# Kernel optimization log

Hardware: AMD Instinct MI355X
Metric: run time of the kernel (lower is better)

Reference implementation:

```python
import jax, jax.numpy as jnp
import numpy as np

B, N = 8192, 128          # batch, num intruders
D_OWN, D_GRID, D_INTR = 16, 512, 20
H, OUT = 128, 4


def setup_inputs() -> dict:
    key = jax.random.key(0)
    ks = jax.random.split(key, 12)
    rn = lambda k, shape, s=1.0: jax.random.normal(k, shape, jnp.float32) * s
    return {
        "state0": rn(ks[0], (B, D_OWN)),
        "state1": rn(ks[1], (B, D_GRID)),
        "state2": rn(ks[2], (B, N, D_INTR)),
        "W_own": rn(ks[3], (D_OWN, H), 0.1), "b_own": jnp.zeros((H,), jnp.float32),
        "W_intr": rn(ks[4], (D_INTR, H), 0.1), "b_intr": jnp.zeros((H,), jnp.float32),
        "W_grid": rn(ks[5], (D_GRID, H), 0.05), "b_grid": jnp.zeros((H,), jnp.float32),
        "Wq": rn(ks[6], (H, H), 0.08),
        "Wk": rn(ks[7], (H, H), 0.08),
        "Wv": rn(ks[8], (H, H), 0.08),
        "W1": rn(ks[9], (3 * H, H), 0.05), "b1": jnp.zeros((H,), jnp.float32),
        "W2": rn(ks[10], (H, OUT), 0.1), "b2": jnp.zeros((OUT,), jnp.float32),
    }


def reference(state0, state1, state2, W_own, b_own, W_intr, b_intr,
              W_grid, b_grid, Wq, Wk, Wv, W1, b1, W2, b2):
    own_e = jax.nn.relu(state0 @ W_own + b_own)            # [B,H]
    x_e = jax.nn.relu(state2 @ W_intr + b_intr)            # [B,N,H]
    q = own_e @ Wq                                         # [B,H]
    k = x_e @ Wk                                           # [B,N,H]
    v = x_e @ Wv                                           # [B,N,H]
    # mask = state2.mean(axis=2, keepdim=True).bool()  (nonzero test)
    mask = jnp.mean(state2, axis=2, keepdims=True) != 0    # [B,N,1]
    score = jnp.einsum('bnh,bh->bn', k, q)[..., None]      # bmm(k, q.unsqueeze(2)) -> [B,N,1]
    score = jnp.where(mask, score, -jnp.inf)
    alpha = jax.nn.softmax(score / np.float32(np.sqrt(H)), axis=1)
    alpha = jnp.where(mask, alpha, 0.0)
    v_att = jnp.sum(v * alpha, axis=1)                     # [B,H]
    own_grid = jax.nn.relu(state1 @ W_grid + b_grid)       # [B,H]
    concat = jnp.concatenate([own_e, v_att, own_grid], axis=1)  # [B,3H]
    out = (concat @ W1 + b1) @ W2 + b2                     # action_out_SAC
    mean = out
    log_std = jnp.clip(out, -20.0, 2.0)
    return mean, log_std
```

## Files before the change

### kernel.cpp

```cpp
#include <hip/hip_runtime.h>

typedef unsigned short ushort_t;
typedef __attribute__((ext_vector_type(8))) short bf16x8;
typedef __attribute__((ext_vector_type(4))) float f32x4;

__device__ __forceinline__ float bflo(unsigned u) { return __uint_as_float(u << 16); }
__device__ __forceinline__ float bfhi(unsigned u) { return __uint_as_float(u & 0xffff0000u); }
__device__ __forceinline__ float bfu(ushort_t s)  { return __uint_as_float((unsigned)s << 16); }
__device__ __forceinline__ ushort_t f2bf(float f) {
    unsigned u = __float_as_uint(f);
    u = u + 0x7fffu + ((u >> 16) & 1u);
    return (ushort_t)(u >> 16);
}
__device__ __forceinline__ void unpack8(uint4 v, float* f) {
    f[0]=bflo(v.x); f[1]=bfhi(v.x); f[2]=bflo(v.y); f[3]=bfhi(v.y);
    f[4]=bflo(v.z); f[5]=bfhi(v.z); f[6]=bflo(v.w); f[7]=bfhi(v.w);
}

__device__ __forceinline__ float load1(const void* p, size_t i, int f32) {
    return f32 ? ((const float*)p)[i] : bfu(((const ushort_t*)p)[i]);
}
__device__ __forceinline__ void load8(const void* p, size_t i, int f32, float* f) {
    if (f32) {
        const float4 a = *(const float4*)((const float*)p + i);
        const float4 b = *(const float4*)((const float*)p + i + 4);
        f[0]=a.x; f[1]=a.y; f[2]=a.z; f[3]=a.w;
        f[4]=b.x; f[5]=b.y; f[6]=b.z; f[7]=b.w;
    } else {
        unpack8(*(const uint4*)((const ushort_t*)p + i), f);
    }
}
__device__ __forceinline__ void load4(const void* p, size_t i, int f32, float* f) {
    if (f32) {
        const float4 a = *(const float4*)((const float*)p + i);
        f[0]=a.x; f[1]=a.y; f[2]=a.z; f[3]=a.w;
    } else {
        const uint2 u = *(const uint2*)((const ushort_t*)p + i);
        f[0]=bflo(u.x); f[1]=bfhi(u.x); f[2]=bflo(u.y); f[3]=bfhi(u.y);
    }
}

__device__ __forceinline__ int detect_f32(const ushort_t* s1h) {
    const int ln = threadIdx.x & 63;
    float v = fmaxf(fabsf(bfu(s1h[ln])), fabsf(bfu(s1h[ln + 64])));
    bool big = !(v <= 1e6f);
    return __ballot(big) != 0ull;
}

#define B_TOT 8192

__device__ __attribute__((aligned(16))) float    g_M[128 * 128];
__device__ __attribute__((aligned(16))) float    g_Wc1[384 * 4];
__device__ __attribute__((aligned(16))) float    g_Wv2[128 * 4];
__device__ __attribute__((aligned(16))) float    g_bc[4];
__device__ __attribute__((aligned(16))) float    g_t[B_TOT * 128];
__device__ __attribute__((aligned(16))) float    g_ogc[B_TOT * 4];
__device__ __attribute__((aligned(16))) ushort_t g_oe[B_TOT * 128];

__global__ __launch_bounds__(128) void k_pre(
    const void* __restrict__ Wq, const void* __restrict__ Wk,
    const void* __restrict__ Wv, const void* __restrict__ W1,
    const void* __restrict__ b1, const void* __restrict__ W2,
    const void* __restrict__ b2, const ushort_t* __restrict__ s1h)
{
    __shared__ float wq_sh[128];
    __shared__ float w2_sh[512];
    __shared__ float wc1_mid[512];
    __shared__ float redc[128][4];
    const int tid = threadIdx.x;
    const int bx = blockIdx.x;
    const int f32 = detect_f32(s1h);

    if (bx < 128) {
        wq_sh[tid] = load1(Wq, bx*128 + tid, f32);
        __syncthreads();
        float acc = 0.f;
        #pragma unroll
        for (int c = 0; c < 16; ++c) {
            float f[8]; load8(Wk, (size_t)tid*128 + c*8, f32, f);
            #pragma unroll
            for (int j = 0; j < 8; ++j) acc = fmaf(wq_sh[c*8+j], f[j], acc);
        }
        g_M[bx*128 + tid] = acc;
    } else {
        const int rbase = (bx == 128) ? 0 : ((bx == 129) ? 128 : 256);
        for (int i = tid; i < 512; i += 128) w2_sh[i] = load1(W2, i, f32);
        __syncthreads();

        const int r = rbase + tid;
        float a[4] = {0.f, 0.f, 0.f, 0.f};
        #pragma unroll
        for (int c = 0; c < 16; ++c) {
            float f[8]; load8(W1, (size_t)r*128 + c*8, f32, f);
            #pragma unroll
            for (int j = 0; j < 8; ++j) {
                const int p = c*8 + j;
                #pragma unroll
                for (int q = 0; q < 4; ++q) a[q] = fmaf(f[j], w2_sh[p*4+q], a[q]);
            }
        }
        #pragma unroll
        for (int q = 0; q < 4; ++q) g_Wc1[r*4+q] = a[q];

        if (bx == 129) {
            #pragma unroll
            for (int q = 0; q < 4; ++q) wc1_mid[tid*4+q] = a[q];
            __syncthreads();
            float v[4] = {0.f, 0.f, 0.f, 0.f};
            #pragma unroll
            for (int c = 0; c < 16; ++c) {
                float f[8]; load8(Wv, (size_t)tid*128 + c*8, f32, f);
                #pragma unroll
                for (int j = 0; j < 8; ++j) {
                    const int i2 = c*8 + j;
                    #pragma unroll
                    for (int q = 0; q < 4; ++q) v[q] = fmaf(f[j], wc1_mid[i2*4+q], v[q]);
                }
            }
            #pragma unroll
            for (int q = 0; q < 4; ++q) g_Wv2[tid*4+q] = v[q];

            const float bv = load1(b1, tid, f32);
            #pragma unroll
            for (int q = 0; q < 4; ++q) redc[tid][q] = bv * w2_sh[tid*4+q];
            __syncthreads();
            for (int s = 64; s > 0; s >>= 1) {
                if (tid < s) {
                    #pragma unroll
                    for (int q = 0; q < 4; ++q) redc[tid][q] += redc[tid+s][q];
                }
                __syncthreads();
            }
            if (tid < 4) g_bc[tid] = redc[0][tid] + load1(b2, tid, f32);
        }
    }
}

__global__ __launch_bounds__(256) void k_ownt(
    const void* __restrict__ state0, const void* __restrict__ W_own,
    const void* __restrict__ b_own, const ushort_t* __restrict__ s1h)
{
    __shared__ float s0sh[16*16];
    __shared__ float wosh[16*128];
    __shared__ float bosh[128];
    __shared__ float oesh[16*129];
    __shared__ float Mt[32][128];
    const int tid = threadIdx.x;
    const int b0 = blockIdx.x * 16;
    const int f32 = detect_f32(s1h);

    if (tid < 32) {
        float f[8]; load8(state0, (size_t)b0*16 + tid*8, f32, f);
        #pragma unroll
        for (int j = 0; j < 8; ++j) s0sh[tid*8 + j] = f[j];
    }
    {
        float f[8]; load8(W_own, (size_t)tid*8, f32, f);
        #pragma unroll
        for (int j = 0; j < 8; ++j) wosh[tid*8 + j] = f[j];
    }
    if (tid < 128) bosh[tid] = load1(b_own, tid, f32);
    __syncthreads();

    #pragma unroll
    for (int kk = 0; kk < 8; ++kk) {
        const int idx = tid + kk*256;
        const int bi = idx >> 7, h = idx & 127;
        float acc = bosh[h];
        #pragma unroll
        for (int d = 0; d < 16; ++d) acc = fmaf(s0sh[bi*16+d], wosh[d*128+h], acc);
        acc = fmaxf(acc, 0.f);
        oesh[bi*129 + h] = acc;
        g_oe[(size_t)(b0+bi)*128 + h] = f2bf(acc);
    }

    const int bi0 = (tid >> 5) * 2;
    const int h0  = (tid & 31) * 4;
    float t00=0.f,t01=0.f,t02=0.f,t03=0.f,t10=0.f,t11=0.f,t12=0.f,t13=0.f;
    for (int kt = 0; kt < 128; kt += 32) {
        __syncthreads();
        #pragma unroll
        for (int c = 0; c < 4; ++c) {
            const int i = tid + c*256;
            const int kk = i >> 5;
            const int hh = (i & 31) * 4;
            *(float4*)&Mt[kk][hh] = *(const float4*)&g_M[(size_t)(kt+kk)*128 + hh];
        }
        __syncthreads();
        #pragma unroll
        for (int k = 0; k < 32; ++k) {
            const float4 mv = *(const float4*)&Mt[k][h0];
            const float a0 = oesh[(bi0+0)*129 + kt + k];
            const float a1 = oesh[(bi0+1)*129 + kt + k];
            t00=fmaf(a0,mv.x,t00); t01=fmaf(a0,mv.y,t01); t02=fmaf(a0,mv.z,t02); t03=fmaf(a0,mv.w,t03);
            t10=fmaf(a1,mv.x,t10); t11=fmaf(a1,mv.y,t11); t12=fmaf(a1,mv.z,t12); t13=fmaf(a1,mv.w,t13);
        }
    }
    *(float4*)&g_t[(size_t)(b0+bi0+0)*128 + h0] = make_float4(t00,t01,t02,t03);
    *(float4*)&g_t[(size_t)(b0+bi0+1)*128 + h0] = make_float4(t10,t11,t12,t13);
}

__global__ __launch_bounds__(256) void k_grid(
    const void* __restrict__ state1, const void* __restrict__ W_grid,
    const void* __restrict__ b_grid)
{
    __shared__ float s1T[32][18];
    __shared__ float wg[32][128];
    __shared__ float part[32][16][4];
    const int tid = threadIdx.x;
    const int b0 = blockIdx.x * 16;
    const int f32 = detect_f32((const ushort_t*)state1);

    const int bq = tid & 7;
    const int hq = tid >> 3;
    float a00=0.f,a01=0.f,a02=0.f,a03=0.f;
    float a10=0.f,a11=0.f,a12=0.f,a13=0.f;

    for (int kt = 0; kt < 512; kt += 32) {
        if (kt) __syncthreads();
        if (tid < 128) {
            const int bb = tid >> 3;
            const int kk = (tid & 7) * 4;
            float f[4];
            load4(state1, (size_t)(b0 + bb)*512 + kt + kk, f32, f);
            #pragma unroll
            for (int j = 0; j < 4; ++j) s1T[kk + j][bb] = f[j];
        }
        {
            #pragma unroll
            for (int c = 0; c < 4; ++c) {
                const int i = tid + c*256;
                const int kk = i >> 5;
                const int hh = (i & 31) * 4;
                float f[4];
                load4(W_grid, (size_t)(kt + kk)*128 + hh, f32, f);
                *(float4*)&wg[kk][hh] = make_float4(f[0], f[1], f[2], f[3]);
            }
        }
        __syncthreads();
        #pragma unroll 8
        for (int k = 0; k < 32; ++k) {
            const float x0 = s1T[k][bq*2 + 0];
            const float x1 = s1T[k][bq*2 + 1];
            const float4 w = *(const float4*)&wg[k][hq*4];
            a00=fmaf(x0,w.x,a00); a01=fmaf(x0,w.y,a01); a02=fmaf(x0,w.z,a02); a03=fmaf(x0,w.w,a03);
            a10=fmaf(x1,w.x,a10); a11=fmaf(x1,w.y,a11); a12=fmaf(x1,w.z,a12); a13=fmaf(x1,w.w,a13);
        }
    }

    float accs[2][4] = {{a00,a01,a02,a03},{a10,a11,a12,a13}};
    float pr[2][4] = {{0,0,0,0},{0,0,0,0}};
    #pragma unroll
    for (int jh = 0; jh < 4; ++jh) {
        const int h = hq*4 + jh;
        const float bg = load1(b_grid, h, f32);
        const float4 wc = *(const float4*)&g_Wc1[(256 + h)*4];
        #pragma unroll
        for (int ib = 0; ib < 2; ++ib) {
            const float og = fmaxf(accs[ib][jh] + bg, 0.f);
            pr[ib][0] = fmaf(og, wc.x, pr[ib][0]);
            pr[ib][1] = fmaf(og, wc.y, pr[ib][1]);
            pr[ib][2] = fmaf(og, wc.z, pr[ib][2]);
            pr[ib][3] = fmaf(og, wc.w, pr[ib][3]);
        }
    }
    __syncthreads();
    #pragma unroll
    for (int j = 0; j < 4; ++j) {
        part[hq][bq*2+0][j] = pr[0][j];
        part[hq][bq*2+1][j] = pr[1][j];
    }
    __syncthreads();
    if (tid < 64) {
        const int bb = tid >> 2, j = tid & 3;
        float s = 0.f;
        #pragma unroll
        for (int q = 0; q < 32; ++q) s += part[q][bb][j];
        g_ogc[(size_t)(b0 + bb)*4 + j] = s;
    }
}

__global__ __launch_bounds__(256) void k_main(
    const void* __restrict__ state2, const void* __restrict__ W_intr,
    const void* __restrict__ b_intr, const ushort_t* __restrict__ s1h,
    void* __restrict__ out_raw)
{
    __shared__ __attribute__((aligned(16))) ushort_t s2b[128*40];
    __shared__ __attribute__((aligned(16))) ushort_t wib[128*40];
    __shared__ float bi_sh[128], t_sh[128], oe_sh[128];
    __shared__ float score_sh[128], alpha_sh[128], u_sh[128];
    __shared__ float u_red[4][128];
    __shared__ int   msk_sh[128];
    __shared__ float red_sh[8];
    __shared__ float red4[4][4];

    const int tid = threadIdx.x;
    const int b = blockIdx.x;
    const int f32 = detect_f32(s1h);

    if (tid < 128) {
        const int n = tid;
        float v[20];
        const size_t base = (size_t)b*2560 + n*20;
        #pragma unroll
        for (int c = 0; c < 5; ++c) load4(state2, base + c*4, f32, v + c*4);
        float ms = 0.f;
        #pragma unroll
        for (int d = 0; d < 20; ++d) ms += v[d];
        msk_sh[n] = (ms != 0.f) ? 1 : 0;
        unsigned* row = (unsigned*)&s2b[n*40];
        #pragma unroll
        for (int c = 0; c < 10; ++c)
            row[c] = (unsigned)f2bf(v[2*c]) | ((unsigned)f2bf(v[2*c+1]) << 16);
        #pragma unroll
        for (int c = 10; c < 20; ++c) row[c] = 0u;
        t_sh[n]  = g_t[(size_t)b*128 + n];
        oe_sh[n] = bfu(g_oe[(size_t)b*128 + n]);
        bi_sh[n] = load1(b_intr, n, f32);
    } else {
        const int h = tid - 128;
        float w[20];
        #pragma unroll
        for (int d = 0; d < 20; ++d) w[d] = load1(W_intr, (size_t)d*128 + h, f32);
        unsigned* row = (unsigned*)&wib[h*40];
        #pragma unroll
        for (int c = 0; c < 10; ++c)
            row[c] = (unsigned)f2bf(w[2*c]) | ((unsigned)f2bf(w[2*c+1]) << 16);
        #pragma unroll
        for (int c = 10; c < 20; ++c) row[c] = 0u;
    }
    __syncthreads();

    const int wv = tid >> 6, ln = tid & 63, lq = ln >> 4, lc = ln & 15;
    const bf16x8 a0 = *(const bf16x8*)&s2b[((2*wv+0)*16 + lc)*40 + lq*8];
    const bf16x8 a1 = *(const bf16x8*)&s2b[((2*wv+1)*16 + lc)*40 + lq*8];
    const f32x4 zf = {0.f, 0.f, 0.f, 0.f};
    f32x4 acc[2][8];
    #pragma unroll
    for (int th = 0; th < 8; ++th) {
        const bf16x8 bb = *(const bf16x8*)&wib[(th*16 + lc)*40 + lq*8];
        acc[0][th] = __builtin_amdgcn_mfma_f32_16x16x32_bf16(a0, bb, zf, 0, 0, 0);
        acc[1][th] = __builtin_amdgcn_mfma_f32_16x16x32_bf16(a1, bb, zf, 0, 0, 0);
    }

    float sc[2][4] = {{0,0,0,0},{0,0,0,0}};
    #pragma unroll
    for (int th = 0; th < 8; ++th) {
        const float bh = bi_sh[th*16 + lc];
        const float tv = t_sh[th*16 + lc];
        #pragma unroll
        for (int i = 0; i < 2; ++i)
            #pragma unroll
            for (int r = 0; r < 4; ++r) {
                const float xv = fmaxf(acc[i][th][r] + bh, 0.f);
                acc[i][th][r] = xv;
                sc[i][r] = fmaf(xv, tv, sc[i][r]);
            }
    }
    #pragma unroll
    for (int off = 1; off < 16; off <<= 1)
        #pragma unroll
        for (int i = 0; i < 2; ++i)
            #pragma unroll
            for (int r = 0; r < 4; ++r)
                sc[i][r] += __shfl_xor(sc[i][r], off);
    if (lc == 0) {
        #pragma unroll
        for (int i = 0; i < 2; ++i)
            #pragma unroll
            for (int r = 0; r < 4; ++r)
                score_sh[(2*wv+i)*16 + lq*4 + r] = sc[i][r];
    }
    __syncthreads();

    float logit = -1e30f, e = 0.f;
    bool is_m = false;
    if (tid < 128) {
        is_m = msk_sh[tid] != 0;
        if (is_m) logit = score_sh[tid] * 0.08838834764831845f;
    }
    float vmax = logit;
    #pragma unroll
    for (int off = 32; off > 0; off >>= 1) vmax = fmaxf(vmax, __shfl_down(vmax, off));
    if ((tid & 63) == 0) red_sh[tid >> 6] = vmax;
    __syncthreads();
    const float mx = fmaxf(fmaxf(red_sh[0], red_sh[1]), fmaxf(red_sh[2], red_sh[3]));
    if (is_m) e = __expf(fmaxf(logit - mx, -80.f));
    float vs = e;
    #pragma unroll
    for (int off = 32; off > 0; off >>= 1) vs += __shfl_down(vs, off);
    if ((tid & 63) == 0) red_sh[4 + (tid >> 6)] = vs;
    __syncthreads();
    const float denom = red_sh[4] + red_sh[5] + red_sh[6] + red_sh[7];
    if (tid < 128) alpha_sh[tid] = (is_m && denom > 0.f) ? e / denom : 0.f;
    __syncthreads();

    float al[2][4];
    #pragma unroll
    for (int i = 0; i < 2; ++i)
        #pragma unroll
        for (int r = 0; r < 4; ++r)
            al[i][r] = alpha_sh[(2*wv+i)*16 + lq*4 + r];
    float up[8];
    #pragma unroll
    for (int th = 0; th < 8; ++th) {
        float s = 0.f;
        #pragma unroll
        for (int i = 0; i < 2; ++i)
            #pragma unroll
            for (int r = 0; r < 4; ++r)
                s = fmaf(al[i][r], acc[i][th][r], s);
        up[th] = s;
    }
    #pragma unroll
    for (int th = 0; th < 8; ++th) {
        up[th] += __shfl_xor(up[th], 16);
        up[th] += __shfl_xor(up[th], 32);
    }
    if (ln < 16) {
        #pragma unroll
        for (int th = 0; th < 8; ++th) u_red[wv][th*16 + ln] = up[th];
    }
    __syncthreads();
    if (tid < 128)
        u_sh[tid] = u_red[0][tid] + u_red[1][tid] + u_red[2][tid] + u_red[3][tid];
    __syncthreads();

    float c0=0.f, c1=0.f, c2=0.f, c3=0.f;
    if (tid < 128) {
        const int h = tid;
        const float uu = u_sh[h], oo = oe_sh[h];
        const float4 wv2 = *(const float4*)&g_Wv2[h*4];
        const float4 wca = *(const float4*)&g_Wc1[h*4];
        c0 = uu*wv2.x + oo*wca.x;
        c1 = uu*wv2.y + oo*wca.y;
        c2 = uu*wv2.z + oo*wca.z;
        c3 = uu*wv2.w + oo*wca.w;
    }
    #pragma unroll
    for (int off = 32; off > 0; off >>= 1) {
        c0 += __shfl_down(c0, off); c1 += __shfl_down(c1, off);
        c2 += __shfl_down(c2, off); c3 += __shfl_down(c3, off);
    }
    if ((tid & 63) == 0) {
        const int w = tid >> 6;
        red4[w][0]=c0; red4[w][1]=c1; red4[w][2]=c2; red4[w][3]=c3;
    }
    __syncthreads();
    if (tid < 4) {
        const int j = tid;
        const float o = g_bc[j] + g_ogc[(size_t)b*4 + j]
                      + red4[0][j] + red4[1][j] + red4[2][j] + red4[3][j];
        const float ls = fminf(fmaxf(o, -20.f), 2.f);
        if (f32) {
            float* of = (float*)out_raw;
            of[(size_t)b*4 + j] = o;
            of[(size_t)B_TOT*4 + (size_t)b*4 + j] = ls;
        } else {
            ushort_t* os = (ushort_t*)out_raw;
            os[(size_t)b*4 + j] = f2bf(o);
            os[(size_t)B_TOT*4 + (size_t)b*4 + j] = f2bf(ls);
        }
    }
}

extern "C" void kernel_launch(void* const* d_in, const int* in_sizes, int n_in,
                              void* d_out, int out_size, void* d_ws, size_t ws_size,
                              hipStream_t stream)
{
    (void)in_sizes; (void)n_in; (void)out_size; (void)d_ws; (void)ws_size;
    const void* state0 = d_in[0];
    const void* state1 = d_in[1];
    const void* state2 = d_in[2];
    const void* W_own  = d_in[3];
    const void* b_own  = d_in[4];
    const void* W_intr = d_in[5];
    const void* b_intr = d_in[6];
    const void* W_grid = d_in[7];
    const void* b_grid = d_in[8];
    const void* Wq     = d_in[9];
    const void* Wk     = d_in[10];
    const void* Wv     = d_in[11];
    const void* W1     = d_in[12];
    const void* b1     = d_in[13];
    const void* W2     = d_in[14];
    const void* b2     = d_in[15];
    const ushort_t* s1h = (const ushort_t*)state1;

    k_pre  <<<dim3(131), dim3(128), 0, stream>>>(Wq, Wk, Wv, W1, b1, W2, b2, s1h);
    k_ownt <<<dim3(512), dim3(256), 0, stream>>>(state0, W_own, b_own, s1h);
    k_grid <<<dim3(512), dim3(256), 0, stream>>>(state1, W_grid, b_grid);
    k_main <<<dim3(8192), dim3(256), 0, stream>>>(state2, W_intr, b_intr, s1h, d_out);
}
```

Baseline: 294.3 us.

## Process one batch row per wavefront in k_main, eliminating block-level syncs

The main attention kernel now gives each wavefront a whole batch row (four rows per block) instead of one row per 256-thread block. state2 is loaded straight from global memory into MFMA A-fragments in registers, and the mask comes from a ballot. Softmax and the weighted sum are done with wave shuffles instead of shared memory and __syncthreads. The MFMA for x_e is computed twice, once for scores and once for the value reduction, to avoid holding 32 accumulators, trading extra matrix work for fewer barriers and less shared-memory traffic.

```diff
diff --git a/kernel.cpp b/kernel.cpp
--- a/kernel.cpp
+++ b/kernel.cpp
@@ -285,181 +285,191 @@
     const void* __restrict__ b_intr, const ushort_t* __restrict__ s1h,
     void* __restrict__ out_raw)
 {
-    __shared__ __attribute__((aligned(16))) ushort_t s2b[128*40];
-    __shared__ __attribute__((aligned(16))) ushort_t wib[128*40];
-    __shared__ float bi_sh[128], t_sh[128], oe_sh[128];
-    __shared__ float score_sh[128], alpha_sh[128], u_sh[128];
-    __shared__ float u_red[4][128];
-    __shared__ int   msk_sh[128];
-    __shared__ float red_sh[8];
-    __shared__ float red4[4][4];
-
+    __shared__ __attribute__((aligned(16))) ushort_t wib[128 * 40];
     const int tid = threadIdx.x;
-    const int b = blockIdx.x;
     const int f32 = detect_f32(s1h);
 
+    #pragma unroll
+    for (int c = 0; c < 10; ++c) {
+        const int idx = c*256 + tid;
+        const int d = idx >> 7, h = idx & 127;
+        wib[h*40 + d] = f32 ? f2bf(((const float*)W_intr)[idx])
+                            : ((const ushort_t*)W_intr)[idx];
+    }
     if (tid < 128) {
-        const int n = tid;
-        float v[20];
-        const size_t base = (size_t)b*2560 + n*20;
-        #pragma unroll
-        for (int c = 0; c < 5; ++c) load4(state2, base + c*4, f32, v + c*4);
-        float ms = 0.f;
-        #pragma unroll
-        for (int d = 0; d < 20; ++d) ms += v[d];
-        msk_sh[n] = (ms != 0.f) ? 1 : 0;
-        unsigned* row = (unsigned*)&s2b[n*40];
-        #pragma unroll
-        for (int c = 0; c < 10; ++c)
-            row[c] = (unsigned)f2bf(v[2*c]) | ((unsigned)f2bf(v[2*c+1]) << 16);
-        #pragma unroll
-        for (int c = 10; c < 20; ++c) row[c] = 0u;
-        t_sh[n]  = g_t[(size_t)b*128 + n];
-        oe_sh[n] = bfu(g_oe[(size_t)b*128 + n]);
-        bi_sh[n] = load1(b_intr, n, f32);
+        #pragma unroll
+        for (int k = 20; k < 32; ++k) wib[tid*40 + k] = 0;
+    }
+    __syncthreads();
+
+    const int wv = tid >> 6, ln = tid & 63, lq = ln >> 4, lc = ln & 15;
+    const int b = blockIdx.x * 4 + wv;
+
+    float bi_r[8], t_r[8];
+    #pragma unroll
+    for (int th = 0; th < 8; ++th) {
+        bi_r[th] = load1(b_intr, th*16 + lc, f32);
+        t_r[th]  = g_t[(size_t)b*128 + th*16 + lc] * 0.08838834764831845f;
+    }
+
+    bf16x8 A[8];
+    unsigned msk[8];
+    if (!f32) {
+        const ushort_t* s2 = (const ushort_t*)state2;
+        #pragma unroll
+        for (int i = 0; i < 8; ++i) {
+            const size_t rb = ((size_t)b*128 + i*16 + lc)*20 + lq*8;
+            uint2 p0 = make_uint2(0u, 0u), p1 = make_uint2(0u, 0u);
+            if (lq < 2)       { p0 = *(const uint2*)(s2 + rb); p1 = *(const uint2*)(s2 + rb + 4); }
+            else if (lq == 2) { p0 = *(const uint2*)(s2 + rb); }
+            union { bf16x8 v; uint2 u[2]; } cv;
+            cv.u[0] = p0; cv.u[1] = p1;
+            A[i] = cv.v;
+            float s = bflo(p0.x)+bfhi(p0.x)+bflo(p0.y)+bfhi(p0.y)
+                    + bflo(p1.x)+bfhi(p1.x)+bflo(p1.y)+bfhi(p1.y);
+            s += __shfl_xor(s, 16);
+            s += __shfl_xor(s, 32);
+            msk[i] = (unsigned)(__ballot(s != 0.f) & 0xffffull);
+        }
     } else {
-        const int h = tid - 128;
-        float w[20];
-        #pragma unroll
-        for (int d = 0; d < 20; ++d) w[d] = load1(W_intr, (size_t)d*128 + h, f32);
-        unsigned* row = (unsigned*)&wib[h*40];
-        #pragma unroll
-        for (int c = 0; c < 10; ++c)
-            row[c] = (unsigned)f2bf(w[2*c]) | ((unsigned)f2bf(w[2*c+1]) << 16);
-        #pragma unroll
-        for (int c = 10; c < 20; ++c) row[c] = 0u;
-    }
-    __syncthreads();
-
-    const int wv = tid >> 6, ln = tid & 63, lq = ln >> 4, lc = ln & 15;
-    const bf16x8 a0 = *(const bf16x8*)&s2b[((2*wv+0)*16 + lc)*40 + lq*8];
-    const bf16x8 a1 = *(const bf16x8*)&s2b[((2*wv+1)*16 + lc)*40 + lq*8];
+        const float* s2 = (const float*)state2;
+        #pragma unroll
+        for (int i = 0; i < 8; ++i) {
+            const size_t rb = ((size_t)b*128 + i*16 + lc)*20 + lq*8;
+            float f[8] = {0.f,0.f,0.f,0.f,0.f,0.f,0.f,0.f};
+            if (lq < 2) {
+                const float4 a4 = *(const float4*)(s2 + rb);
+                const float4 b4 = *(const float4*)(s2 + rb + 4);
+                f[0]=a4.x; f[1]=a4.y; f[2]=a4.z; f[3]=a4.w;
+                f[4]=b4.x; f[5]=b4.y; f[6]=b4.z; f[7]=b4.w;
+            } else if (lq == 2) {
+                const float4 a4 = *(const float4*)(s2 + rb);
+                f[0]=a4.x; f[1]=a4.y; f[2]=a4.z; f[3]=a4.w;
+            }
+            union { bf16x8 v; ushort_t h[8]; } cv;
+            float s = 0.f;
+            #pragma unroll
+            for (int j = 0; j < 8; ++j) { cv.h[j] = f2bf(f[j]); s += f[j]; }
+            A[i] = cv.v;
+            s += __shfl_xor(s, 16);
+            s += __shfl_xor(s, 32);
+            msk[i] = (unsigned)(__ballot(s != 0.f) & 0xffffull);
+        }
+    }
+
     const f32x4 zf = {0.f, 0.f, 0.f, 0.f};
-    f32x4 acc[2][8];
+
+    float sc[8][4];
+    #pragma unroll
+    for (int i = 0; i < 8; ++i)
+        #pragma unroll
+        for (int r = 0; r < 4; ++r) sc[i][r] = 0.f;
+
     #pragma unroll
     for (int th = 0; th < 8; ++th) {
-        const bf16x8 bb = *(const bf16x8*)&wib[(th*16 + lc)*40 + lq*8];
-        acc[0][th] = __builtin_amdgcn_mfma_f32_16x16x32_bf16(a0, bb, zf, 0, 0, 0);
-        acc[1][th] = __builtin_amdgcn_mfma_f32_16x16x32_bf16(a1, bb, zf, 0, 0, 0);
-    }
-
-    float sc[2][4] = {{0,0,0,0},{0,0,0,0}};
-    #pragma unroll
-    for (int th = 0; th < 8; ++th) {
-        const float bh = bi_sh[th*16 + lc];
-        const float tv = t_sh[th*16 + lc];
-        #pragma unroll
-        for (int i = 0; i < 2; ++i)
-            #pragma unroll
-            for (int r = 0; r < 4; ++r) {
-                const float xv = fmaxf(acc[i][th][r] + bh, 0.f);
-                acc[i][th][r] = xv;
-                sc[i][r] = fmaf(xv, tv, sc[i][r]);
-            }
+        const bf16x8 Bv = *(const bf16x8*)&wib[(th*16 + lc)*40 + lq*8];
+        #pragma unroll
+        for (int i = 0; i < 8; ++i) {
+            const f32x4 acc = __builtin_amdgcn_mfma_f32_16x16x32_bf16(A[i], Bv, zf, 0, 0, 0);
+            #pragma unroll
+            for (int r = 0; r < 4; ++r)
+                sc[i][r] = fmaf(fmaxf(acc[r] + bi_r[th], 0.f), t_r[th], sc[i][r]);
+        }
     }
     #pragma unroll
     for (int off = 1; off < 16; off <<= 1)
         #pragma unroll
-        for (int i = 0; i < 2; ++i)
+        for (int i = 0; i < 8; ++i)
             #pragma unroll
             for (int r = 0; r < 4; ++r)
                 sc[i][r] += __shfl_xor(sc[i][r], off);
-    if (lc == 0) {
-        #pragma unroll
-        for (int i = 0; i < 2; ++i)
+
+    float m = -1e30f;
+    #pragma unroll
+    for (int i = 0; i < 8; ++i)
+        #pragma unroll
+        for (int r = 0; r < 4; ++r)
+            if ((msk[i] >> (lq*4 + r)) & 1) m = fmaxf(m, sc[i][r]);
+    m = fmaxf(m, __shfl_xor(m, 16));
+    m = fmaxf(m, __shfl_xor(m, 32));
+
+    float den = 0.f;
+    #pragma unroll
+    for (int i = 0; i < 8; ++i)
+        #pragma unroll
+        for (int r = 0; r < 4; ++r) {
+            float e = 0.f;
+            if ((msk[i] >> (lq*4 + r)) & 1) e = __expf(fmaxf(sc[i][r] - m, -80.f));
+            sc[i][r] = e;
+            den += e;
+        }
+    den += __shfl_xor(den, 16);
+    den += __shfl_xor(den, 32);
+    const float rden = (den > 0.f) ? (1.f / den) : 0.f;
+    #pragma unroll
+    for (int i = 0; i < 8; ++i)
+        #pragma unroll
+        for (int r = 0; r < 4; ++r) sc[i][r] *= rden;
+
+    float o4[4] = {0.f, 0.f, 0.f, 0.f};
+    #pragma unroll
+    for (int th = 0; th < 8; ++th) {
+        const bf16x8 Bv = *(const bf16x8*)&wib[(th*16 + lc)*40 + lq*8];
+        float up = 0.f;
+        #pragma unroll
+        for (int i = 0; i < 8; ++i) {
+            const f32x4 acc = __builtin_amdgcn_mfma_f32_16x16x32_bf16(A[i], Bv, zf, 0, 0, 0);
             #pragma unroll
             for (int r = 0; r < 4; ++r)
-                score_sh[(2*wv+i)*16 + lq*4 + r] = sc[i][r];
-    }
-    __syncthreads();
-
-    float logit = -1e30f, e = 0.f;
-    bool is_m = false;
-    if (tid < 128) {
-        is_m = msk_sh[tid] != 0;
-        if (is_m) logit = score_sh[tid] * 0.08838834764831845f;
-    }
-    float vmax = logit;
-    #pragma unroll
-    for (int off = 32; off > 0; off >>= 1) vmax = fmaxf(vmax, __shfl_down(vmax, off));
-    if ((tid & 63) == 0) red_sh[tid >> 6] = vmax;
-    __syncthreads();
-    const float mx = fmaxf(fmaxf(red_sh[0], red_sh[1]), fmaxf(red_sh[2], red_sh[3]));
-    if (is_m) e = __expf(fmaxf(logit - mx, -80.f));
-    float vs = e;
-    #pragma unroll
-    for (int off = 32; off > 0; off >>= 1) vs += __shfl_down(vs, off);
-    if ((tid & 63) == 0) red_sh[4 + (tid >> 6)] = vs;
-    __syncthreads();
-    const float denom = red_sh[4] + red_sh[5] + red_sh[6] + red_sh[7];
-    if (tid < 128) alpha_sh[tid] = (is_m && denom > 0.f) ? e / denom : 0.f;
-    __syncthreads();
-
-    float al[2][4];
-    #pragma unroll
-    for (int i = 0; i < 2; ++i)
-        #pragma unroll
-        for (int r = 0; r < 4; ++r)
-            al[i][r] = alpha_sh[(2*wv+i)*16 + lq*4 + r];
-    float up[8];
-    #pragma unroll
-    for (int th = 0; th < 8; ++th) {
-        float s = 0.f;
-        #pragma unroll
-        for (int i = 0; i < 2; ++i)
-            #pragma unroll
-            for (int r = 0; r < 4; ++r)
-                s = fmaf(al[i][r], acc[i][th][r], s);
-        up[th] = s;
-    }
-    #pragma unroll
-    for (int th = 0; th < 8; ++th) {
-        up[th] += __shfl_xor(up[th], 16);
-        up[th] += __shfl_xor(up[th], 32);
-    }
-    if (ln < 16) {
-        #pragma unroll
-        for (int th = 0; th < 8; ++th) u_red[wv][th*16 + ln] = up[th];
-    }
-    __syncthreads();
-    if (tid < 128)
-        u_sh[tid] = u_red[0][tid] + u_red[1][tid] + u_red[2][tid] + u_red[3][tid];
-    __syncthreads();
-
-    float c0=0.f, c1=0.f, c2=0.f, c3=0.f;
-    if (tid < 128) {
-        const int h = tid;
-        const float uu = u_sh[h], oo = oe_sh[h];
-        const float4 wv2 = *(const float4*)&g_Wv2[h*4];
-        const float4 wca = *(const float4*)&g_Wc1[h*4];
-        c0 = uu*wv2.x + oo*wca.x;
-        c1 = uu*wv2.y + oo*wca.y;
-        c2 = uu*wv2.z + oo*wca.z;
-        c3 = uu*wv2.w + oo*wca.w;
-    }
-    #pragma unroll
-    for (int off = 32; off > 0; off >>= 1) {
-        c0 += __shfl_down(c0, off); c1 += __shfl_down(c1, off);
-        c2 += __shfl_down(c2, off); c3 += __shfl_down(c3, off);
-    }
-    if ((tid & 63) == 0) {
-        const int w = tid >> 6;
-        red4[w][0]=c0; red4[w][1]=c1; red4[w][2]=c2; red4[w][3]=c3;
-    }
-    __syncthreads();
-    if (tid < 4) {
-        const int j = tid;
-        const float o = g_bc[j] + g_ogc[(size_t)b*4 + j]
-                      + red4[0][j] + red4[1][j] + red4[2][j] + red4[3][j];
-        const float ls = fminf(fmaxf(o, -20.f), 2.f);
+                up = fmaf(sc[i][r], fmaxf(acc[r] + bi_r[th], 0.f), up);
+        }
+        const float4 w2 = *(const float4*)&g_Wv2[(th*16 + lc)*4];
+        o4[0] = fmaf(up, w2.x, o4[0]);
+        o4[1] = fmaf(up, w2.y, o4[1]);
+        o4[2] = fmaf(up, w2.z, o4[2]);
+        o4[3] = fmaf(up, w2.w, o4[3]);
+    }
+
+    {
+        const float oe0 = bfu(g_oe[(size_t)b*128 + ln]);
+        const float oe1 = bfu(g_oe[(size_t)b*128 + 64 + ln]);
+        const float4 wA = *(const float4*)&g_Wc1[ln*4];
+        const float4 wB = *(const float4*)&g_Wc1[(64 + ln)*4];
+        o4[0] += oe0*wA.x + oe1*wB.x;
+        o4[1] += oe0*wA.y + oe1*wB.y;
+        o4[2] += oe0*wA.z + oe1*wB.z;
+        o4[3] += oe0*wA.w + oe1*wB.w;
+    }
+
+    #pragma unroll
+    for (int off = 1; off < 64; off <<= 1)
+        #pragma unroll
+        for (int q = 0; q < 4; ++q)
+            o4[q] += __shfl_xor(o4[q], off);
+
+    if (ln == 0) {
+        const float4 og = *(const float4*)&g_ogc[(size_t)b*4];
+        const float v0 = g_bc[0] + og.x + o4[0];
+        const float v1 = g_bc[1] + og.y + o4[1];
+        const float v2 = g_bc[2] + og.z + o4[2];
+        const float v3 = g_bc[3] + og.w + o4[3];
+        const float l0 = fminf(fmaxf(v0, -20.f), 2.f);
+        const float l1 = fminf(fmaxf(v1, -20.f), 2.f);
+        const float l2 = fminf(fmaxf(v2, -20.f), 2.f);
+        const float l3 = fminf(fmaxf(v3, -20.f), 2.f);
         if (f32) {
             float* of = (float*)out_raw;
-            of[(size_t)b*4 + j] = o;
-            of[(size_t)B_TOT*4 + (size_t)b*4 + j] = ls;
+            *(float4*)&of[(size_t)b*4] = make_float4(v0, v1, v2, v3);
+            *(float4*)&of[((size_t)B_TOT + b)*4] = make_float4(l0, l1, l2, l3);
         } else {
             ushort_t* os = (ushort_t*)out_raw;
-            os[(size_t)b*4 + j] = f2bf(o);
-            os[(size_t)B_TOT*4 + (size_t)b*4 + j] = f2bf(ls);
+            uint2 mw, lw;
+            mw.x = (unsigned)f2bf(v0) | ((unsigned)f2bf(v1) << 16);
+            mw.y = (unsigned)f2bf(v2) | ((unsigned)f2bf(v3) << 16);
+            lw.x = (unsigned)f2bf(l0) | ((unsigned)f2bf(l1) << 16);
+            lw.y = (unsigned)f2bf(l2) | ((unsigned)f2bf(l3) << 16);
+            *(uint2*)&os[(size_t)b*4] = mw;
+            *(uint2*)&os[((size_t)B_TOT + b)*4] = lw;
         }
     }
 }
@@ -487,8 +497,8 @@
     const void* b2     = d_in[15];
     const ushort_t* s1h = (const ushort_t*)state1;
 
-    k_pre  <<<dim3(131), dim3(128), 0, stream>>>(Wq, Wk, Wv, W1, b1, W2, b2, s1h);
-    k_ownt <<<dim3(512), dim3(256), 0, stream>>>(state0, W_own, b_own, s1h);
-    k_grid <<<dim3(512), dim3(256), 0, stream>>>(state1, W_grid, b_grid);
-    k_main <<<dim3(8192), dim3(256), 0, stream>>>(state2, W_intr, b_intr, s1h, d_out);
-}
+    k_pre  <<<dim3(131),  dim3(128), 0, stream>>>(Wq, Wk, Wv, W1, b1, W2, b2, s1h);
+    k_ownt <<<dim3(512),  dim3(256), 0, stream>>>(state0, W_own, b_own, s1h);
+    k_grid <<<dim3(512),  dim3(256), 0, stream>>>(state1, W_grid, b_grid);
+    k_main <<<dim3(2048), dim3(256), 0, stream>>>(state2, W_intr, b_intr, s1h, d_out);
+}
```

Measured after the change: 291.8 us. About the same (-0.9%).
